# Kernel tuning notes

Measured on AMD Instinct MI355X. Metric: run time of the kernel, lower is better.

## Reference

```python
import jax, jax.numpy as jnp
import numpy as np
import itertools

NUM_HEADS = 8
KEY_DIM = 32
ATTN_D = 128  # attn_ratio * key_dim
BN_EPS = 1e-5


def _build_idxs(rx=16, rz=8, tn=1):
    points = list(itertools.product(range(rx), range(rx)))
    for i in range(tn):
        points += list(itertools.product(range(rx + rz * i, rx + rz * (i + 1)),
                                         range(rx + rz * i, rx + rz * (i + 1))))
    offsets = {}
    idxs = []
    for p1 in points:
        for p2 in points:
            off = (abs(p1[0] - p2[0]), abs(p1[1] - p2[1]))
            if off not in offsets:
                offsets[off] = len(offsets)
            idxs.append(offsets[off])
    N = len(points)
    return np.asarray(idxs, dtype=np.int64).reshape(N, N), len(offsets)


def _bn_train(x2d, gamma, beta):
    # BatchNorm1d in training mode: batch mean / biased variance over dim 0
    m = jnp.mean(x2d, axis=0)
    v = jnp.var(x2d, axis=0)
    return (x2d - m) * jax.lax.rsqrt(v + BN_EPS) * gamma + beta


def setup_inputs() -> dict:
    key = jax.random.key(0)
    ks = jax.random.split(key, 4)
    idxs_np, n_off = _build_idxs()  # (320,320), 560
    B, N, C = 128, idxs_np.shape[0], 256
    h = NUM_HEADS * (2 * KEY_DIM + ATTN_D)  # 1536
    dh = NUM_HEADS * ATTN_D  # 1024
    return {
        "x": jax.random.normal(ks[0], (B, N, C), dtype=jnp.float32),
        "Wqkv": jax.random.normal(ks[1], (h, C), dtype=jnp.float32) * 0.02,
        "g1": jnp.ones((h,), jnp.float32),
        "b1": jnp.zeros((h,), jnp.float32),
        "ab": jax.random.normal(ks[2], (NUM_HEADS, n_off), dtype=jnp.float32) * 0.02,
        "Wproj": jax.random.normal(ks[3], (C, dh), dtype=jnp.float32) * 0.02,
        "g2": jnp.ones((C,), jnp.float32),
        "b2": jnp.zeros((C,), jnp.float32),
        "idxs": jnp.asarray(idxs_np),
    }


def reference(x, Wqkv, g1, b1, ab, Wproj, g2, b2, idxs):
    B, N, C = x.shape
    scale = KEY_DIM ** -0.5
    # qkv projection (Linear no-bias) + BatchNorm1d over flattened (B*N, h)
    qkv = jnp.einsum('bnc,hc->bnh', x, Wqkv)
    qkv = _bn_train(qkv.reshape(B * N, -1), g1, b1).reshape(B, N, NUM_HEADS, 2 * KEY_DIM + ATTN_D)
    q = qkv[..., :KEY_DIM]
    k = qkv[..., KEY_DIM:2 * KEY_DIM]
    v = qkv[..., 2 * KEY_DIM:]
    bias = ab[:, idxs]  # gather -> (H, N, N)
    attn = jnp.einsum('bnhd,bmhd->bhnm', q, k) * scale + bias[None]
    attn = jax.nn.softmax(attn, axis=-1)
    out = jnp.einsum('bhnm,bmhd->bnhd', attn, v).reshape(B, N, NUM_HEADS * ATTN_D)
    out = jax.nn.gelu(out, approximate=False)  # activation() before proj
    out = jnp.einsum('bnd,cd->bnc', out, Wproj)
    out = _bn_train(out.reshape(B * N, -1), g2, b2).reshape(B, N, C)
    return out
```

## Files before the change

### kernel.cpp

```cpp
#include <hip/hip_runtime.h>
#include <hip/hip_bf16.h>

#define B_ 128
#define N_ 320
#define C_ 256
#define H_ 8
#define HQKV 1536
#define DH 1024
#define MROWS 40960
#define EPS 1e-5f
#define SCALE 0.17677669529663687f
#define LOG2E 1.4426950408889634f

typedef __attribute__((ext_vector_type(4))) float f32x4;
typedef __attribute__((ext_vector_type(8))) short short8_t;
typedef __attribute__((ext_vector_type(4))) short short4_t;

__device__ inline float bf2f(unsigned short u) { return __uint_as_float(((unsigned)u) << 16); }
__device__ inline unsigned short f2bf(float f) {
    unsigned u = __float_as_uint(f);
    u += 0x7FFF + ((u >> 16) & 1);
    return (unsigned short)(u >> 16);
}

__device__ inline float gelu_f(float v) {
    float v2 = v * v;
    float w = fmaf(v2, 0.044715f, 1.0f);
    float z = v * w * (-2.3022098f);
    float e = __builtin_amdgcn_exp2f(z);
    return v * __builtin_amdgcn_rcpf(1.0f + e);
}

#define GLD16(gp, lp)                                                                  \
    __builtin_amdgcn_global_load_lds((const __attribute__((address_space(1))) void*)(gp), \
                                     (__attribute__((address_space(3))) void*)(lp), 16, 0, 0)

__global__ void conv_all(const float* __restrict__ x, const float* __restrict__ wqkv,
                         const float* __restrict__ wproj, unsigned short* __restrict__ xb,
                         unsigned short* __restrict__ wqb, unsigned short* __restrict__ wpb) {
    int i = blockIdx.x * 256 + threadIdx.x;
    const float* src;
    unsigned short* dst;
    int off;
    if (i < 2621440) { src = x; dst = xb; off = i; }
    else if (i < 2719744) { src = wqkv; dst = wqb; off = i - 2621440; }
    else if (i < 2785280) { src = wproj; dst = wpb; off = i - 2719744; }
    else return;
    f32x4 v = ((const f32x4*)src)[off];
    short4_t o;
#pragma unroll
    for (int j = 0; j < 4; ++j) o[j] = (short)f2bf(v[j]);
    ((short4_t*)dst)[off] = o;
}

__global__ __launch_bounds__(256) void gemm_qkv(const unsigned short* __restrict__ A,
                                                const unsigned short* __restrict__ Bm,
                                                unsigned short* __restrict__ qkB,
                                                unsigned short* __restrict__ vT,
                                                float* __restrict__ sum1, float* __restrict__ sumsq1) {
    __shared__ unsigned short lA[128 * 32];
    __shared__ unsigned short lB[128 * 32];
    const int tid = threadIdx.x;
    const int lane = tid & 63, wid = tid >> 6;
    const int wm = wid >> 1, wn = wid & 1;
    const int lr = lane & 15, g = lane >> 4, lk = g * 8;
    const int m0 = blockIdx.y * 128, n0 = blockIdx.x * 128;
    const int wb0 = tid & 192;
    f32x4 acc[4][4] = {};
    for (int k0 = 0; k0 < 256; k0 += 32) {
        __syncthreads();
#pragma unroll
        for (int j = 0; j < 2; ++j) {
            int idx = j * 256 + tid;
            int wb = j * 256 + wb0;
            GLD16(&A[(size_t)(m0 + (idx >> 2)) * 256 + k0 + (idx & 3) * 8], &lA[(size_t)wb * 8]);
            GLD16(&Bm[(size_t)(n0 + (idx >> 2)) * 256 + k0 + (idx & 3) * 8], &lB[(size_t)wb * 8]);
        }
        __syncthreads();
        short8_t af[4], bfr[4];
#pragma unroll
        for (int i = 0; i < 4; ++i) af[i] = *(short8_t*)&lA[(wm * 64 + i * 16 + lr) * 32 + lk];
#pragma unroll
        for (int j = 0; j < 4; ++j) bfr[j] = *(short8_t*)&lB[(wn * 64 + j * 16 + lr) * 32 + lk];
#pragma unroll
        for (int i = 0; i < 4; ++i)
#pragma unroll
            for (int j = 0; j < 4; ++j)
                acc[i][j] = __builtin_amdgcn_mfma_f32_16x16x32_bf16(af[i], bfr[j], acc[i][j], 0, 0, 0);
    }
    int hhj[4], cmj[4];
#pragma unroll
    for (int j = 0; j < 4; ++j) {
        int col = n0 + wn * 64 + j * 16 + lr;
        hhj[j] = col / 192;
        cmj[j] = col - hhj[j] * 192;
    }
    float cs[4] = {0.f, 0.f, 0.f, 0.f}, css[4] = {0.f, 0.f, 0.f, 0.f};
#pragma unroll
    for (int i = 0; i < 4; ++i) {
        int rowbase = m0 + wm * 64 + i * 16 + g * 4;
        int bq = rowbase / 320;
        int n = rowbase - bq * 320;
#pragma unroll
        for (int j = 0; j < 4; ++j) {
            float v0 = acc[i][j][0], v1 = acc[i][j][1], v2 = acc[i][j][2], v3 = acc[i][j][3];
            cs[j] += (v0 + v1) + (v2 + v3);
            css[j] += (v0 * v0 + v1 * v1) + (v2 * v2 + v3 * v3);
            if (cmj[j] < 64) {
                unsigned short* qp = &qkB[((size_t)(bq * 8 + hhj[j]) * 320 + n) * 64 + cmj[j]];
                qp[0] = f2bf(v0); qp[64] = f2bf(v1); qp[128] = f2bf(v2); qp[192] = f2bf(v3);
            } else {
                short4_t o;
                o[0] = (short)f2bf(v0); o[1] = (short)f2bf(v1);
                o[2] = (short)f2bf(v2); o[3] = (short)f2bf(v3);
                *(short4_t*)&vT[((size_t)(bq * 8 + hhj[j]) * 128 + (cmj[j] - 64)) * 320 + n] = o;
            }
        }
    }
    __syncthreads();
    float* red_s = (float*)lA;
    float* red_ss = (float*)lB;
#pragma unroll
    for (int j = 0; j < 4; ++j) {
        int c = wn * 64 + j * 16 + lr;
        red_s[(wm * 4 + g) * 128 + c] = cs[j];
        red_ss[(wm * 4 + g) * 128 + c] = css[j];
    }
    __syncthreads();
    if (tid < 128) {
        float s = 0.f;
#pragma unroll
        for (int u = 0; u < 8; ++u) s += red_s[u * 128 + tid];
        atomicAdd(&sum1[n0 + tid], s);
    } else {
        int c = tid - 128;
        float s = 0.f;
#pragma unroll
        for (int u = 0; u < 8; ++u) s += red_ss[u * 128 + c];
        atomicAdd(&sumsq1[n0 + c], s);
    }
}

__global__ __launch_bounds__(256) void gemm_proj(const unsigned short* __restrict__ A,
                                                 const unsigned short* __restrict__ Bm,
                                                 float* __restrict__ Cout,
                                                 float* __restrict__ sum2, float* __restrict__ sumsq2) {
    __shared__ unsigned short lA[64 * 32];
    __shared__ unsigned short lB[128 * 32];
    const int tid = threadIdx.x;
    const int lane = tid & 63, wid = tid >> 6;
    const int wm = wid >> 1, wn = wid & 1;
    const int lr = lane & 15, g = lane >> 4, lk = g * 8;
    const int m0 = blockIdx.y * 64, n0 = blockIdx.x * 128;
    const int wb0 = tid & 192;
    f32x4 acc[2][4] = {};
    for (int k0 = 0; k0 < 1024; k0 += 32) {
        __syncthreads();
        GLD16(&A[(size_t)(m0 + (tid >> 2)) * 1024 + k0 + (tid & 3) * 8], &lA[(size_t)wb0 * 8]);
        GLD16(&Bm[(size_t)(n0 + (tid >> 2)) * 1024 + k0 + (tid & 3) * 8], &lB[(size_t)wb0 * 8]);
        GLD16(&Bm[(size_t)(n0 + 64 + (tid >> 2)) * 1024 + k0 + (tid & 3) * 8], &lB[2048 + (size_t)wb0 * 8]);
        __syncthreads();
        short8_t af[2], bfr[4];
#pragma unroll
        for (int i = 0; i < 2; ++i) af[i] = *(short8_t*)&lA[(wm * 32 + i * 16 + lr) * 32 + lk];
#pragma unroll
        for (int j = 0; j < 4; ++j) bfr[j] = *(short8_t*)&lB[(wn * 64 + j * 16 + lr) * 32 + lk];
#pragma unroll
        for (int i = 0; i < 2; ++i)
#pragma unroll
            for (int j = 0; j < 4; ++j)
                acc[i][j] = __builtin_amdgcn_mfma_f32_16x16x32_bf16(af[i], bfr[j], acc[i][j], 0, 0, 0);
    }
    float cs[4] = {0.f, 0.f, 0.f, 0.f}, css[4] = {0.f, 0.f, 0.f, 0.f};
#pragma unroll
    for (int i = 0; i < 2; ++i) {
#pragma unroll
        for (int r = 0; r < 4; ++r) {
            int row = m0 + wm * 32 + i * 16 + g * 4 + r;
#pragma unroll
            for (int j = 0; j < 4; ++j) {
                float val = acc[i][j][r];
                cs[j] += val;
                css[j] += val * val;
                Cout[(size_t)row * 256 + n0 + wn * 64 + j * 16 + lr] = val;
            }
        }
    }
    __syncthreads();
    float* red_s = (float*)lB;
    float* red_ss = (float*)lB + 1024;
#pragma unroll
    for (int j = 0; j < 4; ++j) {
        int c = wn * 64 + j * 16 + lr;
        red_s[(wm * 4 + g) * 128 + c] = cs[j];
        red_ss[(wm * 4 + g) * 128 + c] = css[j];
    }
    __syncthreads();
    if (tid < 128) {
        float s = 0.f;
#pragma unroll
        for (int u = 0; u < 8; ++u) s += red_s[u * 128 + tid];
        atomicAdd(&sum2[n0 + tid], s);
    } else {
        int c = tid - 128;
        float s = 0.f;
#pragma unroll
        for (int u = 0; u < 8; ++u) s += red_ss[u * 128 + c];
        atomicAdd(&sumsq2[n0 + c], s);
    }
}

__global__ void bn_finalize(const float* __restrict__ sum, const float* __restrict__ sumsq,
                            const float* __restrict__ g, const float* __restrict__ b,
                            float* __restrict__ scale, float* __restrict__ shift, int C, float invM) {
    int c = blockIdx.x * 256 + threadIdx.x;
    if (c < C) {
        float mean = sum[c] * invM;
        float var = sumsq[c] * invM - mean * mean;
        float sc = g[c] * rsqrtf(var + EPS);
        scale[c] = sc;
        shift[c] = b[c] - mean * sc;
    }
}

__global__ void prep_w(const float* __restrict__ scale1, const float* __restrict__ shift1,
                       float* __restrict__ wq, float* __restrict__ w2) {
    int c = threadIdx.x;
    if (c < 256) {
        int h = c >> 5, cc = c & 31;
        int qch = h * 192 + cc, kch = qch + 32;
        wq[c] = scale1[qch] * scale1[kch] * (SCALE * LOG2E);
        w2[c] = shift1[qch] * scale1[kch] * (SCALE * LOG2E);
    }
}

__global__ void uk_kernel(const unsigned short* __restrict__ qkB, const float* __restrict__ w2,
                          float* __restrict__ uk) {
    int idx = blockIdx.x * 256 + threadIdx.x;
    if (idx < 128 * 8 * 320) {
        int bh = idx / 320;
        int h = bh & 7;
        const unsigned short* kp = &qkB[(size_t)idx * 64 + 32];
        float s = 0.f;
#pragma unroll
        for (int c4 = 0; c4 < 4; ++c4) {
            short8_t kk = *(const short8_t*)&kp[c4 * 8];
#pragma unroll
            for (int j = 0; j < 8; ++j) s += bf2f((unsigned short)kk[j]) * w2[(h << 5) + c4 * 8 + j];
        }
        uk[idx] = s;
    }
}

__global__ void bias_build(const float* __restrict__ ab, const int* __restrict__ idxs,
                           unsigned short* __restrict__ biasb, int n_off) {
    int i = blockIdx.x * 256 + threadIdx.x;
    if (i < H_ * N_ * N_) {
        int h = i / (N_ * N_);
        int r = i % (N_ * N_);
        biasb[i] = f2bf(ab[h * n_off + idxs[r]] * LOG2E);
    }
}

__global__ __launch_bounds__(256) void attn_kernel(const unsigned short* __restrict__ qkB,
                                                   const unsigned short* __restrict__ vT,
                                                   const float* __restrict__ wq,
                                                   const float* __restrict__ uk,
                                                   const unsigned short* __restrict__ biasb,
                                                   const float* __restrict__ scale1,
                                                   const float* __restrict__ shift1,
                                                   unsigned short* __restrict__ attnout) {
    __shared__ unsigned short Plds[4][10][16][40];
    __shared__ float sums[64];
    const int tid = threadIdx.x;
    const int lane = tid & 63, wid = tid >> 6;
    const int lr = lane & 15, g = lane >> 4;
    const int h = blockIdx.x;
    const int b = blockIdx.y / 5, qt = blockIdx.y % 5;
    const int bh = b * 8 + h;

    int qrow = qt * 64 + wid * 16 + lr;
    short8_t qraw = *(const short8_t*)&qkB[((size_t)bh * 320 + qrow) * 64 + g * 8];
    short8_t aq;
#pragma unroll
    for (int j = 0; j < 8; ++j)
        aq[j] = (short)f2bf(bf2f((unsigned short)qraw[j]) * wq[(h << 5) + g * 8 + j]);

    const unsigned short* Kbase = &qkB[(size_t)bh * 320 * 64 + 32 + g * 8];
    f32x4 sacc[20];
#pragma unroll
    for (int t = 0; t < 20; ++t) {
        short8_t bk = *(const short8_t*)&Kbase[(size_t)(t * 16 + lr) * 64];
        f32x4 z = {};
        sacc[t] = __builtin_amdgcn_mfma_f32_16x16x32_bf16(aq, bk, z, 0, 0, 0);
    }

    const int nloc0 = qt * 64 + wid * 16 + g * 4;
    const unsigned short* biasrow = &biasb[(size_t)h * 102400];
    const float* ukrow = &uk[(size_t)bh * 320];
    float sumr[4] = {0.f, 0.f, 0.f, 0.f};
#pragma unroll
    for (int t = 0; t < 20; ++t) {
        float ukv = ukrow[t * 16 + lr];
#pragma unroll
        for (int r = 0; r < 4; ++r) {
            float s = sacc[t][r] + ukv + bf2f(biasrow[(size_t)(nloc0 + r) * 320 + t * 16 + lr]);
            float p = __builtin_amdgcn_exp2f(s);
            sumr[r] += p;
            Plds[wid][t >> 1][g * 4 + r][(t & 1) * 16 + lr] = f2bf(p);
        }
    }
#pragma unroll
    for (int r = 0; r < 4; ++r) {
#pragma unroll
        for (int ms = 1; ms < 16; ms <<= 1) sumr[r] += __shfl_xor(sumr[r], ms);
        if (lr == 0) sums[wid * 16 + g * 4 + r] = sumr[r];
    }
    __syncthreads();

    const unsigned short* Vb = &vT[(size_t)bh * 128 * 320 + g * 8];
    f32x4 oacc[4][2] = {};
#pragma unroll
    for (int t = 0; t < 10; ++t) {
        short8_t bv0 = *(const short8_t*)&Vb[(size_t)(wid * 32 + lr) * 320 + t * 32];
        short8_t bv1 = *(const short8_t*)&Vb[(size_t)(wid * 32 + 16 + lr) * 320 + t * 32];
#pragma unroll
        for (int qw = 0; qw < 4; ++qw) {
            short8_t ap = *(short8_t*)&Plds[qw][t][lr][g * 8];
            oacc[qw][0] = __builtin_amdgcn_mfma_f32_16x16x32_bf16(ap, bv0, oacc[qw][0], 0, 0, 0);
            oacc[qw][1] = __builtin_amdgcn_mfma_f32_16x16x32_bf16(ap, bv1, oacc[qw][1], 0, 0, 0);
        }
    }

    float svv[2], tvv[2];
#pragma unroll
    for (int dtl = 0; dtl < 2; ++dtl) {
        int ch = h * 192 + 64 + wid * 32 + dtl * 16 + lr;
        svv[dtl] = scale1[ch];
        tvv[dtl] = shift1[ch];
    }
#pragma unroll
    for (int qw = 0; qw < 4; ++qw) {
#pragma unroll
        for (int r = 0; r < 4; ++r) {
            float inv = __builtin_amdgcn_rcpf(sums[qw * 16 + g * 4 + r]);
            size_t nrow = (size_t)b * 320 + qt * 64 + qw * 16 + g * 4 + r;
#pragma unroll
            for (int dtl = 0; dtl < 2; ++dtl) {
                float v = oacc[qw][dtl][r] * inv * svv[dtl] + tvv[dtl];
                attnout[nrow * 1024 + h * 128 + wid * 32 + dtl * 16 + lr] = f2bf(gelu_f(v));
            }
        }
    }
}

__global__ void bn_apply(float* __restrict__ out, const float* __restrict__ scale,
                         const float* __restrict__ shift) {
    int i = blockIdx.x * 256 + threadIdx.x;
    const int total = MROWS * C_ / 4;
    for (; i < total; i += gridDim.x * 256) {
        f32x4 v = *(const f32x4*)&out[(size_t)i * 4];
        int c = (i * 4) & 255;
        f32x4 o;
#pragma unroll
        for (int j = 0; j < 4; ++j) o[j] = v[j] * scale[c + j] + shift[c + j];
        *(f32x4*)&out[(size_t)i * 4] = o;
    }
}

extern "C" void kernel_launch(void* const* d_in, const int* in_sizes, int n_in,
                              void* d_out, int out_size, void* d_ws, size_t ws_size,
                              hipStream_t stream) {
    const float* x = (const float*)d_in[0];
    const float* Wqkv = (const float*)d_in[1];
    const float* g1 = (const float*)d_in[2];
    const float* b1 = (const float*)d_in[3];
    const float* ab = (const float*)d_in[4];
    const float* Wproj = (const float*)d_in[5];
    const float* g2 = (const float*)d_in[6];
    const float* b2 = (const float*)d_in[7];
    const int* idxs = (const int*)d_in[8];
    const int n_off = in_sizes[4] / H_;

    char* ws = (char*)d_ws;
    unsigned short* qkB = (unsigned short*)ws;
    unsigned short* vT = (unsigned short*)(ws + 41943040);
    unsigned short* attnout = (unsigned short*)(ws + 125829120);
    unsigned short* xb = attnout;
    unsigned short* biasb = (unsigned short*)(ws + 209715200);
    float* uk = (float*)(ws + 212992000);
    unsigned short* wqb = (unsigned short*)(ws + 214302720);
    unsigned short* wpb = (unsigned short*)(ws + 215089152);
    float* stats = (float*)(ws + 215613440);
    float* sum1 = stats;
    float* sumsq1 = stats + 1536;
    float* sum2 = stats + 3072;
    float* sumsq2 = sum2 + 256;
    float* scale1 = sumsq2 + 256;
    float* shift1 = scale1 + 1536;
    float* scale2 = shift1 + 1536;
    float* shift2 = scale2 + 256;
    float* wq = shift2 + 256;
    float* w2 = wq + 256;

    hipMemsetAsync(stats, 0, 3584 * 4, stream);
    conv_all<<<dim3(10880), 256, 0, stream>>>(x, Wqkv, Wproj, xb, wqb, wpb);
    bias_build<<<dim3(3200), 256, 0, stream>>>(ab, idxs, biasb, n_off);
    gemm_qkv<<<dim3(12, 320), 256, 0, stream>>>(xb, wqb, qkB, vT, sum1, sumsq1);
    bn_finalize<<<dim3(6), 256, 0, stream>>>(sum1, sumsq1, g1, b1, scale1, shift1, 1536, 1.0f / MROWS);
    prep_w<<<dim3(1), 256, 0, stream>>>(scale1, shift1, wq, w2);
    uk_kernel<<<dim3(1280), 256, 0, stream>>>(qkB, w2, uk);
    attn_kernel<<<dim3(8, 640), 256, 0, stream>>>(qkB, vT, wq, uk, biasb, scale1, shift1, attnout);
    gemm_proj<<<dim3(2, 640), 256, 0, stream>>>(attnout, wpb, (float*)d_out, sum2, sumsq2);
    bn_finalize<<<dim3(1), 256, 0, stream>>>(sum2, sumsq2, g2, b2, scale2, shift2, 256, 1.0f / MROWS);
    bn_apply<<<dim3(2048), 256, 0, stream>>>((float*)d_out, scale2, shift2);
}
```

Before: 301.7 us.

## Double-buffer GEMM LDS loads, swizzle qkv grid, fuse small BN prep kernels

Both GEMMs now use two LDS buffers, so the next K-slice's global-to-LDS loads are issued while MFMAs run on the current one, with one barrier per iteration instead of two. The qkv GEMM also remaps block IDs so neighbouring blocks share tiles and get better L2 reuse. The prep_w and second bn_finalize kernels are folded into their consumers (uk_kernel, attn_kernel, bn_apply), which saves launches. The attention MFMA sections get raised wave priority via s_setprio. The double buffers double LDS use, which may lower occupancy, and an unused f2bf2 helper is added.

```diff
diff --git a/kernel.cpp b/kernel.cpp
--- a/kernel.cpp
+++ b/kernel.cpp
@@ -21,6 +21,10 @@
     unsigned u = __float_as_uint(f);
     u += 0x7FFF + ((u >> 16) & 1);
     return (unsigned short)(u >> 16);
+}
+__device__ inline unsigned int f2bf2(float a, float b) {
+    __hip_bfloat162 h2 = __float22bfloat162_rn(make_float2(a, b));
+    return *(unsigned int*)&h2;
 }
 
 __device__ inline float gelu_f(float v) {
@@ -58,30 +62,39 @@
                                                 unsigned short* __restrict__ qkB,
                                                 unsigned short* __restrict__ vT,
                                                 float* __restrict__ sum1, float* __restrict__ sumsq1) {
-    __shared__ unsigned short lA[128 * 32];
-    __shared__ unsigned short lB[128 * 32];
+    __shared__ unsigned short lA[2][128 * 32];
+    __shared__ unsigned short lB[2][128 * 32];
     const int tid = threadIdx.x;
     const int lane = tid & 63, wid = tid >> 6;
     const int wm = wid >> 1, wn = wid & 1;
     const int lr = lane & 15, g = lane >> 4, lk = g * 8;
-    const int m0 = blockIdx.y * 128, n0 = blockIdx.x * 128;
+    const int orig = blockIdx.y * 12 + blockIdx.x;
+    const int id2 = (orig & 7) * 480 + (orig >> 3);
+    const int m0 = (id2 / 12) * 128, n0 = (id2 % 12) * 128;
     const int wb0 = tid & 192;
+    const int srow = tid >> 2, scg = (tid & 3) * 8;
+
+#define STAGE_QKV(it, buf)                                                               \
+    {                                                                                    \
+        int k0 = (it) * 32;                                                              \
+        GLD16(&A[(size_t)(m0 + srow) * 256 + k0 + scg], &lA[buf][(size_t)wb0 * 8]);      \
+        GLD16(&Bm[(size_t)(n0 + srow) * 256 + k0 + scg], &lB[buf][(size_t)wb0 * 8]);     \
+        GLD16(&A[(size_t)(m0 + 64 + srow) * 256 + k0 + scg], &lA[buf][2048 + (size_t)wb0 * 8]); \
+        GLD16(&Bm[(size_t)(n0 + 64 + srow) * 256 + k0 + scg], &lB[buf][2048 + (size_t)wb0 * 8]); \
+    }
+
+    STAGE_QKV(0, 0);
     f32x4 acc[4][4] = {};
-    for (int k0 = 0; k0 < 256; k0 += 32) {
+    for (int it = 0; it < 8; ++it) {
         __syncthreads();
-#pragma unroll
-        for (int j = 0; j < 2; ++j) {
-            int idx = j * 256 + tid;
-            int wb = j * 256 + wb0;
-            GLD16(&A[(size_t)(m0 + (idx >> 2)) * 256 + k0 + (idx & 3) * 8], &lA[(size_t)wb * 8]);
-            GLD16(&Bm[(size_t)(n0 + (idx >> 2)) * 256 + k0 + (idx & 3) * 8], &lB[(size_t)wb * 8]);
-        }
-        __syncthreads();
+        if (it < 7) STAGE_QKV(it + 1, (it + 1) & 1);
+        const unsigned short* la = lA[it & 1];
+        const unsigned short* lb = lB[it & 1];
         short8_t af[4], bfr[4];
 #pragma unroll
-        for (int i = 0; i < 4; ++i) af[i] = *(short8_t*)&lA[(wm * 64 + i * 16 + lr) * 32 + lk];
-#pragma unroll
-        for (int j = 0; j < 4; ++j) bfr[j] = *(short8_t*)&lB[(wn * 64 + j * 16 + lr) * 32 + lk];
+        for (int i = 0; i < 4; ++i) af[i] = *(const short8_t*)&la[(wm * 64 + i * 16 + lr) * 32 + lk];
+#pragma unroll
+        for (int j = 0; j < 4; ++j) bfr[j] = *(const short8_t*)&lb[(wn * 64 + j * 16 + lr) * 32 + lk];
 #pragma unroll
         for (int i = 0; i < 4; ++i)
 #pragma unroll
@@ -145,26 +158,36 @@
                                                  const unsigned short* __restrict__ Bm,
                                                  float* __restrict__ Cout,
                                                  float* __restrict__ sum2, float* __restrict__ sumsq2) {
-    __shared__ unsigned short lA[64 * 32];
-    __shared__ unsigned short lB[128 * 32];
+    __shared__ unsigned short lA[2][64 * 32];
+    __shared__ unsigned short lB[2][128 * 32];
     const int tid = threadIdx.x;
     const int lane = tid & 63, wid = tid >> 6;
     const int wm = wid >> 1, wn = wid & 1;
     const int lr = lane & 15, g = lane >> 4, lk = g * 8;
     const int m0 = blockIdx.y * 64, n0 = blockIdx.x * 128;
     const int wb0 = tid & 192;
+    const int srow = tid >> 2, scg = (tid & 3) * 8;
+
+#define STAGE_PROJ(it, buf)                                                              \
+    {                                                                                    \
+        int k0 = (it) * 32;                                                              \
+        GLD16(&A[(size_t)(m0 + srow) * 1024 + k0 + scg], &lA[buf][(size_t)wb0 * 8]);     \
+        GLD16(&Bm[(size_t)(n0 + srow) * 1024 + k0 + scg], &lB[buf][(size_t)wb0 * 8]);    \
+        GLD16(&Bm[(size_t)(n0 + 64 + srow) * 1024 + k0 + scg], &lB[buf][2048 + (size_t)wb0 * 8]); \
+    }
+
+    STAGE_PROJ(0, 0);
     f32x4 acc[2][4] = {};
-    for (int k0 = 0; k0 < 1024; k0 += 32) {
+    for (int it = 0; it < 32; ++it) {
         __syncthreads();
-        GLD16(&A[(size_t)(m0 + (tid >> 2)) * 1024 + k0 + (tid & 3) * 8], &lA[(size_t)wb0 * 8]);
-        GLD16(&Bm[(size_t)(n0 + (tid >> 2)) * 1024 + k0 + (tid & 3) * 8], &lB[(size_t)wb0 * 8]);
-        GLD16(&Bm[(size_t)(n0 + 64 + (tid >> 2)) * 1024 + k0 + (tid & 3) * 8], &lB[2048 + (size_t)wb0 * 8]);
-        __syncthreads();
+        if (it < 31) STAGE_PROJ(it + 1, (it + 1) & 1);
+        const unsigned short* la = lA[it & 1];
+        const unsigned short* lb = lB[it & 1];
         short8_t af[2], bfr[4];
 #pragma unroll
-        for (int i = 0; i < 2; ++i) af[i] = *(short8_t*)&lA[(wm * 32 + i * 16 + lr) * 32 + lk];
-#pragma unroll
-        for (int j = 0; j < 4; ++j) bfr[j] = *(short8_t*)&lB[(wn * 64 + j * 16 + lr) * 32 + lk];
+        for (int i = 0; i < 2; ++i) af[i] = *(const short8_t*)&la[(wm * 32 + i * 16 + lr) * 32 + lk];
+#pragma unroll
+        for (int j = 0; j < 4; ++j) bfr[j] = *(const short8_t*)&lb[(wn * 64 + j * 16 + lr) * 32 + lk];
 #pragma unroll
         for (int i = 0; i < 2; ++i)
 #pragma unroll
@@ -223,19 +246,16 @@
     }
 }
 
-__global__ void prep_w(const float* __restrict__ scale1, const float* __restrict__ shift1,
-                       float* __restrict__ wq, float* __restrict__ w2) {
-    int c = threadIdx.x;
-    if (c < 256) {
-        int h = c >> 5, cc = c & 31;
-        int qch = h * 192 + cc, kch = qch + 32;
-        wq[c] = scale1[qch] * scale1[kch] * (SCALE * LOG2E);
-        w2[c] = shift1[qch] * scale1[kch] * (SCALE * LOG2E);
-    }
-}
-
-__global__ void uk_kernel(const unsigned short* __restrict__ qkB, const float* __restrict__ w2,
-                          float* __restrict__ uk) {
+__global__ void uk_kernel(const unsigned short* __restrict__ qkB, const float* __restrict__ scale1,
+                          const float* __restrict__ shift1, float* __restrict__ uk) {
+    __shared__ float w2l[256];
+    {
+        int c = threadIdx.x;
+        int hh = c >> 5, cc = c & 31;
+        int qch = hh * 192 + cc;
+        w2l[c] = shift1[qch] * scale1[qch + 32] * (SCALE * LOG2E);
+    }
+    __syncthreads();
     int idx = blockIdx.x * 256 + threadIdx.x;
     if (idx < 128 * 8 * 320) {
         int bh = idx / 320;
@@ -246,7 +266,7 @@
         for (int c4 = 0; c4 < 4; ++c4) {
             short8_t kk = *(const short8_t*)&kp[c4 * 8];
 #pragma unroll
-            for (int j = 0; j < 8; ++j) s += bf2f((unsigned short)kk[j]) * w2[(h << 5) + c4 * 8 + j];
+            for (int j = 0; j < 8; ++j) s += bf2f((unsigned short)kk[j]) * w2l[(h << 5) + c4 * 8 + j];
         }
         uk[idx] = s;
     }
@@ -264,7 +284,6 @@
 
 __global__ __launch_bounds__(256) void attn_kernel(const unsigned short* __restrict__ qkB,
                                                    const unsigned short* __restrict__ vT,
-                                                   const float* __restrict__ wq,
                                                    const float* __restrict__ uk,
                                                    const unsigned short* __restrict__ biasb,
                                                    const float* __restrict__ scale1,
@@ -282,18 +301,23 @@
     int qrow = qt * 64 + wid * 16 + lr;
     short8_t qraw = *(const short8_t*)&qkB[((size_t)bh * 320 + qrow) * 64 + g * 8];
     short8_t aq;
-#pragma unroll
-    for (int j = 0; j < 8; ++j)
-        aq[j] = (short)f2bf(bf2f((unsigned short)qraw[j]) * wq[(h << 5) + g * 8 + j]);
+    const int cq = h * 192 + g * 8;
+#pragma unroll
+    for (int j = 0; j < 8; ++j) {
+        float w = scale1[cq + j] * scale1[cq + 32 + j] * (SCALE * LOG2E);
+        aq[j] = (short)f2bf(bf2f((unsigned short)qraw[j]) * w);
+    }
 
     const unsigned short* Kbase = &qkB[(size_t)bh * 320 * 64 + 32 + g * 8];
     f32x4 sacc[20];
+    __builtin_amdgcn_s_setprio(1);
 #pragma unroll
     for (int t = 0; t < 20; ++t) {
         short8_t bk = *(const short8_t*)&Kbase[(size_t)(t * 16 + lr) * 64];
         f32x4 z = {};
         sacc[t] = __builtin_amdgcn_mfma_f32_16x16x32_bf16(aq, bk, z, 0, 0, 0);
     }
+    __builtin_amdgcn_s_setprio(0);
 
     const int nloc0 = qt * 64 + wid * 16 + g * 4;
     const unsigned short* biasrow = &biasb[(size_t)h * 102400];
@@ -320,6 +344,7 @@
 
     const unsigned short* Vb = &vT[(size_t)bh * 128 * 320 + g * 8];
     f32x4 oacc[4][2] = {};
+    __builtin_amdgcn_s_setprio(1);
 #pragma unroll
     for (int t = 0; t < 10; ++t) {
         short8_t bv0 = *(const short8_t*)&Vb[(size_t)(wid * 32 + lr) * 320 + t * 32];
@@ -331,6 +356,7 @@
             oacc[qw][1] = __builtin_amdgcn_mfma_f32_16x16x32_bf16(ap, bv1, oacc[qw][1], 0, 0, 0);
         }
     }
+    __builtin_amdgcn_s_setprio(0);
 
     float svv[2], tvv[2];
 #pragma unroll
@@ -354,8 +380,19 @@
     }
 }
 
-__global__ void bn_apply(float* __restrict__ out, const float* __restrict__ scale,
-                         const float* __restrict__ shift) {
+__global__ void bn_apply(float* __restrict__ out, const float* __restrict__ sum2,
+                         const float* __restrict__ sumsq2, const float* __restrict__ g2,
+                         const float* __restrict__ b2) {
+    __shared__ float sc[256], sh[256];
+    {
+        int c = threadIdx.x;
+        float mean = sum2[c] * (1.0f / MROWS);
+        float var = sumsq2[c] * (1.0f / MROWS) - mean * mean;
+        float s = g2[c] * rsqrtf(var + EPS);
+        sc[c] = s;
+        sh[c] = b2[c] - mean * s;
+    }
+    __syncthreads();
     int i = blockIdx.x * 256 + threadIdx.x;
     const int total = MROWS * C_ / 4;
     for (; i < total; i += gridDim.x * 256) {
@@ -363,7 +400,7 @@
         int c = (i * 4) & 255;
         f32x4 o;
 #pragma unroll
-        for (int j = 0; j < 4; ++j) o[j] = v[j] * scale[c + j] + shift[c + j];
+        for (int j = 0; j < 4; ++j) o[j] = v[j] * sc[c + j] + sh[c + j];
         *(f32x4*)&out[(size_t)i * 4] = o;
     }
 }
@@ -398,20 +435,14 @@
     float* sumsq2 = sum2 + 256;
     float* scale1 = sumsq2 + 256;
     float* shift1 = scale1 + 1536;
-    float* scale2 = shift1 + 1536;
-    float* shift2 = scale2 + 256;
-    float* wq = shift2 + 256;
-    float* w2 = wq + 256;
 
     hipMemsetAsync(stats, 0, 3584 * 4, stream);
     conv_all<<<dim3(10880), 256, 0, stream>>>(x, Wqkv, Wproj, xb, wqb, wpb);
     bias_build<<<dim3(3200), 256, 0, stream>>>(ab, idxs, biasb, n_off);
     gemm_qkv<<<dim3(12, 320), 256, 0, stream>>>(xb, wqb, qkB, vT, sum1, sumsq1);
     bn_finalize<<<dim3(6), 256, 0, stream>>>(sum1, sumsq1, g1, b1, scale1, shift1, 1536, 1.0f / MROWS);
-    prep_w<<<dim3(1), 256, 0, stream>>>(scale1, shift1, wq, w2);
-    uk_kernel<<<dim3(1280), 256, 0, stream>>>(qkB, w2, uk);
-    attn_kernel<<<dim3(8, 640), 256, 0, stream>>>(qkB, vT, wq, uk, biasb, scale1, shift1, attnout);
+    uk_kernel<<<dim3(1280), 256, 0, stream>>>(qkB, scale1, shift1, uk);
+    attn_kernel<<<dim3(8, 640), 256, 0, stream>>>(qkB, vT, uk, biasb, scale1, shift1, attnout);
     gemm_proj<<<dim3(2, 640), 256, 0, stream>>>(attnout, wpb, (float*)d_out, sum2, sumsq2);
-    bn_finalize<<<dim3(1), 256, 0, stream>>>(sum2, sumsq2, g2, b2, scale2, shift2, 256, 1.0f / MROWS);
-    bn_apply<<<dim3(2048), 256, 0, stream>>>((float*)d_out, scale2, shift2);
-}
+    bn_apply<<<dim3(2048), 256, 0, stream>>>((float*)d_out, sum2, sumsq2, g2, b2);
+}
```

After: 287.8 us. -4.6%, faster.
